# Optimization experiments

Hardware: AMD Instinct MI355X
Metric: run time of the kernel (lower is better)

## Reference

```python
import jax, jax.numpy as jnp
import numpy as np

MODES = 16
IN_CH = 64
OUT_CH = 64
SCALE = 1.0 / (IN_CH * OUT_CH)


def setup_inputs() -> dict:
    key = jax.random.key(0)
    k1, k2, k3 = jax.random.split(key, 3)
    v = jax.random.normal(k1, (32, IN_CH, 8192), dtype=jnp.float32)
    # torch.rand on cfloat -> uniform [0,1) real and imag parts, then scaled
    w_real = jax.random.uniform(k2, (MODES, OUT_CH, IN_CH), dtype=jnp.float32) * SCALE
    w_imag = jax.random.uniform(k3, (MODES, OUT_CH, IN_CH), dtype=jnp.float32) * SCALE
    return {"v": v, "w_real": w_real, "w_imag": w_imag}


def reference(v, w_real, w_imag):
    # v: [B, Cin, N]; weights: [modes, Cout, Cin] complex
    W = w_real + 1j * w_imag
    vf = jnp.fft.rfft(v)                      # [B, Cin, Nf], complex64
    nf = vf.shape[-1]
    # 'koi,bki->bko' with bki = vf[:,:, :modes] transposed -> equivalently:
    lv = jnp.einsum('koi,bik->bok', W, vf[:, :, :MODES])  # [B, Cout, modes]
    lv_full = jnp.pad(lv, ((0, 0), (0, 0), (0, nf - MODES)))  # zero high modes
    return jnp.fft.irfft(lv_full, n=v.shape[-1])  # [B, Cout, N] real
```

## Files before the change

kernel.cpp:

```cpp
#include <hip/hip_runtime.h>
#include <math.h>

#define NN 8192
#define NMODES 16
#define NB 32
#define NCH 64
#define NROWS (NB * NCH)
#define TPB 256

#define K8 0.70710678118654752440f

typedef float f32x4 __attribute__((ext_vector_type(4)));

struct KCTab { float c[16][4]; float s[16][4]; };
constexpr KCTab make_kc() {
  KCTab r{};
  for (int k = 0; k < 16; ++k)
    for (int c = 0; c < 4; ++c) {
      double th = 6.283185307179586476925287 * (double)(k * c) / 8192.0;
      double x2 = th * th;
      r.c[k][c] = (float)(1.0 - x2 / 2.0 + x2 * x2 / 24.0 - x2 * x2 * x2 / 720.0);
      r.s[k][c] = (float)(th - th * x2 / 6.0 + th * x2 * x2 / 120.0 - th * x2 * x2 * x2 / 5040.0);
    }
  return r;
}
constexpr KCTab KCT = make_kc();

__global__ __launch_bounds__(TPB) void fwd_dft_kernel(
    const float* __restrict__ v, float* __restrict__ vfpart) {
  const int row = blockIdx.x;
  const int t = threadIdx.x;
  const f32x4* __restrict__ vr4 = (const f32x4*)(v + (size_t)row * NN);

  float x[4][8];
#pragma unroll
  for (int j = 0; j < 8; ++j) {
    const f32x4 q = vr4[t + TPB * j];
    x[0][j] = q.x; x[1][j] = q.y; x[2][j] = q.z; x[3][j] = q.w;
  }

  float X0[4], X4[4], X1r[4], X1i[4], X2r[4], X2i[4], X3r[4], X3i[4];
#pragma unroll
  for (int c = 0; c < 4; ++c) {
    const float a  = x[c][0] + x[c][4], b = x[c][0] - x[c][4];
    const float cc = x[c][2] + x[c][6], d = x[c][2] - x[c][6];
    const float e  = x[c][1] + x[c][5], f = x[c][1] - x[c][5];
    const float g  = x[c][3] + x[c][7], h = x[c][3] - x[c][7];
    const float t1 = a + cc, t2 = e + g;
    X0[c]  = t1 + t2;
    X4[c]  = t1 - t2;
    X2r[c] = a - cc;  X2i[c] = g - e;
    const float u = K8 * (f - h), w = K8 * (f + h);
    X1r[c] = b + u;   X1i[c] = -d - w;
    X3r[c] = b - u;   X3i[c] = d - w;
  }

  double phi = (double)t * (6.283185307179586476925287 / 2048.0);
  double spd, cpd;
  sincos(phi, &spd, &cpd);
  const float c1 = (float)cpd, s1 = (float)spd;

  float pr[NMODES], pi[NMODES];
  float ck = 1.f, sk = 0.f;
#pragma unroll
  for (int k = 0; k < NMODES; ++k) {
    const int m = k & 7;
    float ar = 0.f, ai = 0.f;
#pragma unroll
    for (int c = 0; c < 4; ++c) {
      float br, bi;
      switch (m) {
        case 0:  br = X0[c];  bi = 0.f;      break;
        case 1:  br = X1r[c]; bi = X1i[c];   break;
        case 2:  br = X2r[c]; bi = X2i[c];   break;
        case 3:  br = X3r[c]; bi = X3i[c];   break;
        case 4:  br = X4[c];  bi = 0.f;      break;
        case 5:  br = X3r[c]; bi = -X3i[c];  break;
        case 6:  br = X2r[c]; bi = -X2i[c];  break;
        default: br = X1r[c]; bi = -X1i[c];  break;
      }
      if (c == 0) { ar = br; ai = bi; }
      else {
        ar = fmaf(br, KCT.c[k][c], fmaf(bi,  KCT.s[k][c], ar));
        ai = fmaf(bi, KCT.c[k][c], fmaf(br, -KCT.s[k][c], ai));
      }
    }
    pr[k] = ar * ck + ai * sk;
    pi[k] = ai * ck - ar * sk;
    const float cn = ck * c1 - sk * s1;
    const float sn = sk * c1 + ck * s1;
    ck = cn; sk = sn;
  }

  const int lane = t & 63, wave = t >> 6;

  float u16[16];
  {
    const bool hi = (lane & 16) != 0;
#pragma unroll
    for (int i = 0; i < 16; ++i) {
      const float send = hi ? pr[i] : pi[i];
      const float recv = __shfl_xor(send, 16);
      u16[i] = (hi ? pi[i] : pr[i]) + recv;
    }
  }
  float u8[8];
  {
    const bool hi = (lane & 8) != 0;
#pragma unroll
    for (int i = 0; i < 8; ++i) {
      const float send = hi ? u16[i] : u16[i + 8];
      const float recv = __shfl_xor(send, 8);
      u8[i] = (hi ? u16[i + 8] : u16[i]) + recv;
    }
  }
  float u4[4];
  {
    const bool hi = (lane & 4) != 0;
#pragma unroll
    for (int i = 0; i < 4; ++i) {
      const float send = hi ? u8[i] : u8[i + 4];
      const float recv = __shfl_xor(send, 4);
      u4[i] = (hi ? u8[i + 4] : u8[i]) + recv;
    }
  }
  float u2[2];
  {
    const bool hi = (lane & 2) != 0;
#pragma unroll
    for (int i = 0; i < 2; ++i) {
      const float send = hi ? u4[i] : u4[i + 2];
      const float recv = __shfl_xor(send, 2);
      u2[i] = (hi ? u4[i + 2] : u4[i]) + recv;
    }
  }
  float u1;
  {
    const bool hi = (lane & 1) != 0;
    const float send = hi ? u2[0] : u2[1];
    const float recv = __shfl_xor(send, 1);
    u1 = (hi ? u2[1] : u2[0]) + recv;
  }
  const float total = u1 + __shfl_xor(u1, 32);

  if (lane < 32) {
    vfpart[((size_t)row * 4 + wave) * 32 + lane] = total;
  }
}

__global__ __launch_bounds__(TPB) void mix_inv_kernel(
    const float* __restrict__ vfpart, const float* __restrict__ wre,
    const float* __restrict__ wim, float* __restrict__ out) {
  const int bid = blockIdx.x;
  const int b = bid >> 6, o = bid & 63;
  const int t = threadIdx.x;

  __shared__ float red[16][33];
  __shared__ float lvs[32];

  {
    const int k = t & 15, g = t >> 4;
    float lr = 0.f, li = 0.f;
#pragma unroll
    for (int ii = 0; ii < 4; ++ii) {
      const int i = g * 4 + ii;
      const float* __restrict__ p = vfpart + (size_t)(b * NCH + i) * 128;
      float vr = 0.f, vi = 0.f;
#pragma unroll
      for (int w = 0; w < 4; ++w) {
        vr += p[w * 32 + k];
        vi += p[w * 32 + 16 + k];
      }
      const float wr = wre[((size_t)k * NCH + o) * NCH + i];
      const float wi = wim[((size_t)k * NCH + o) * NCH + i];
      lr = fmaf(wr, vr, fmaf(-wi, vi, lr));
      li = fmaf(wr, vi, fmaf( wi, vr, li));
    }
    red[g][k]      = lr;
    red[g][16 + k] = li;
  }
  __syncthreads();
  if (t < 32) {
    float s = 0.f;
#pragma unroll
    for (int g = 0; g < 16; ++g) s += red[g][t];
    const float gk = ((t & 15) == 0) ? (1.0f / (float)NN) : (2.0f / (float)NN);
    lvs[t] = s * gk;
  }
  __syncthreads();

  double phi = (double)t * (6.283185307179586476925287 / 2048.0);
  double spd, cpd;
  sincos(phi, &spd, &cpd);
  const float c1 = (float)cpd, s1 = (float)spd;

  float Er[4][8], Ei[4][8];
  {
    float ck = 1.f, sk = 0.f;
#pragma unroll
    for (int k = 0; k < NMODES; ++k) {
      const int m = k & 7;
      const float Ar = lvs[k], Ai = lvs[16 + k];
      const float xr = Ar * ck - Ai * sk;
      const float xi = Ai * ck + Ar * sk;
      if (k < 8) { Er[0][m] = xr; Ei[0][m] = xi; }
      else       { Er[0][m] += xr; Ei[0][m] += xi; }
#pragma unroll
      for (int c = 1; c < 4; ++c) {
        const float dr = fmaf(xr, KCT.c[k][c], -xi * KCT.s[k][c]);
        const float di = fmaf(xi, KCT.c[k][c],  xr * KCT.s[k][c]);
        if (k < 8) { Er[c][m] = dr; Ei[c][m] = di; }
        else       { Er[c][m] += dr; Ei[c][m] += di; }
      }
      const float cn = ck * c1 - sk * s1;
      const float sn = sk * c1 + ck * s1;
      ck = cn; sk = sn;
    }
  }

  float y[4][8];
#pragma unroll
  for (int c = 0; c < 4; ++c) {
    const float P0 = Er[c][0], P4 = Er[c][4];
    const float P1 = Er[c][1] + Er[c][7], Q1 = Ei[c][1] - Ei[c][7];
    const float P2 = Er[c][2] + Er[c][6], Q2 = Ei[c][2] - Ei[c][6];
    const float P3 = Er[c][3] + Er[c][5], Q3 = Ei[c][3] - Ei[c][5];
    const float s04 = P0 + P4, d04 = P0 - P4;
    const float e0 = s04 + P2, e2 = s04 - P2;
    const float e1 = d04 - Q2, e3 = d04 + Q2;
    const float alpha = P1 - P3, beta = Q1 + Q3;
    const float O0 = P1 + P3;
    const float O2 = Q3 - Q1;
    const float O1 =  K8 * (alpha - beta);
    const float O3 = -K8 * (alpha + beta);
    y[c][0] = e0 + O0; y[c][4] = e0 - O0;
    y[c][1] = e1 + O1; y[c][5] = e1 - O1;
    y[c][2] = e2 + O2; y[c][6] = e2 - O2;
    y[c][3] = e3 + O3; y[c][7] = e3 - O3;
  }

  f32x4* __restrict__ out4 = (f32x4*)(out + (size_t)bid * NN);
#pragma unroll
  for (int j = 0; j < 8; ++j) {
    f32x4 r;
    r.x = y[0][j]; r.y = y[1][j]; r.z = y[2][j]; r.w = y[3][j];
    out4[t + TPB * j] = r;
  }
}

extern "C" void kernel_launch(void* const* d_in, const int* in_sizes, int n_in,
                              void* d_out, int out_size, void* d_ws, size_t ws_size,
                              hipStream_t stream) {
  const float* v   = (const float*)d_in[0];
  const float* wre = (const float*)d_in[1];
  const float* wim = (const float*)d_in[2];
  float* out = (float*)d_out;

  float* vfpart = (float*)d_ws;

  fwd_dft_kernel<<<NROWS, TPB, 0, stream>>>(v, vfpart);
  mix_inv_kernel<<<NROWS, TPB, 0, stream>>>(vfpart, wre, wim, out);
}
```

Before: 31.88 us.

## Split mode mixing into separate kernel before inverse DFT

Moves the channel-mixing contraction out of the fused mix+inverse kernel into its own small kernel (128 blocks, one thread per output channel and mode, looping over all 64 input channels), writing the mixed spectrum to a workspace buffer. The inverse DFT kernel then reads 32 floats per row directly instead of recomputing the mix with a shared-memory reduction and two barriers per block. This removes the redundant per-block reduction and barriers but adds a third kernel launch, a serial 64-step loop with strided weight loads, and a global round trip for the mixed spectrum.

```diff
diff --git a/kernel.cpp b/kernel.cpp
--- a/kernel.cpp
+++ b/kernel.cpp
@@ -148,46 +148,39 @@
   }
 }
 
-__global__ __launch_bounds__(TPB) void mix_inv_kernel(
+__global__ __launch_bounds__(256) void mix_kernel(
     const float* __restrict__ vfpart, const float* __restrict__ wre,
-    const float* __restrict__ wim, float* __restrict__ out) {
+    const float* __restrict__ wim, float* __restrict__ lv) {
+  const int k   = threadIdx.x & 15;
+  const int olo = threadIdx.x >> 4;
+  const int b   = blockIdx.x >> 2;
+  const int o   = (blockIdx.x & 3) * 16 + olo;
+
+  float lr = 0.f, li = 0.f;
+  for (int i = 0; i < NCH; ++i) {
+    const float* __restrict__ p = vfpart + (size_t)(b * NCH + i) * 128;
+    float vr = 0.f, vi = 0.f;
+#pragma unroll
+    for (int w = 0; w < 4; ++w) {
+      vr += p[w * 32 + k];
+      vi += p[w * 32 + 16 + k];
+    }
+    const float wr = wre[((size_t)k * NCH + o) * NCH + i];
+    const float wi = wim[((size_t)k * NCH + o) * NCH + i];
+    lr = fmaf(wr, vr, fmaf(-wi, vi, lr));
+    li = fmaf(wr, vi, fmaf( wi, vr, li));
+  }
+  const float gk = (k == 0) ? (1.0f / (float)NN) : (2.0f / (float)NN);
+  float* dst = lv + (size_t)(b * NCH + o) * 32;
+  dst[k]      = lr * gk;
+  dst[16 + k] = li * gk;
+}
+
+__global__ __launch_bounds__(TPB) void inv_kernel(
+    const float* __restrict__ lv, float* __restrict__ out) {
   const int bid = blockIdx.x;
-  const int b = bid >> 6, o = bid & 63;
   const int t = threadIdx.x;
-
-  __shared__ float red[16][33];
-  __shared__ float lvs[32];
-
-  {
-    const int k = t & 15, g = t >> 4;
-    float lr = 0.f, li = 0.f;
-#pragma unroll
-    for (int ii = 0; ii < 4; ++ii) {
-      const int i = g * 4 + ii;
-      const float* __restrict__ p = vfpart + (size_t)(b * NCH + i) * 128;
-      float vr = 0.f, vi = 0.f;
-#pragma unroll
-      for (int w = 0; w < 4; ++w) {
-        vr += p[w * 32 + k];
-        vi += p[w * 32 + 16 + k];
-      }
-      const float wr = wre[((size_t)k * NCH + o) * NCH + i];
-      const float wi = wim[((size_t)k * NCH + o) * NCH + i];
-      lr = fmaf(wr, vr, fmaf(-wi, vi, lr));
-      li = fmaf(wr, vi, fmaf( wi, vr, li));
-    }
-    red[g][k]      = lr;
-    red[g][16 + k] = li;
-  }
-  __syncthreads();
-  if (t < 32) {
-    float s = 0.f;
-#pragma unroll
-    for (int g = 0; g < 16; ++g) s += red[g][t];
-    const float gk = ((t & 15) == 0) ? (1.0f / (float)NN) : (2.0f / (float)NN);
-    lvs[t] = s * gk;
-  }
-  __syncthreads();
+  const float* __restrict__ L = lv + (size_t)bid * 32;
 
   double phi = (double)t * (6.283185307179586476925287 / 2048.0);
   double spd, cpd;
@@ -200,7 +193,7 @@
 #pragma unroll
     for (int k = 0; k < NMODES; ++k) {
       const int m = k & 7;
-      const float Ar = lvs[k], Ai = lvs[16 + k];
+      const float Ar = L[k], Ai = L[16 + k];
       const float xr = Ar * ck - Ai * sk;
       const float xi = Ai * ck + Ar * sk;
       if (k < 8) { Er[0][m] = xr; Ei[0][m] = xi; }
@@ -257,7 +250,9 @@
   float* out = (float*)d_out;
 
   float* vfpart = (float*)d_ws;
+  float* lvbuf  = vfpart + (size_t)NROWS * 4 * 32;
 
   fwd_dft_kernel<<<NROWS, TPB, 0, stream>>>(v, vfpart);
-  mix_inv_kernel<<<NROWS, TPB, 0, stream>>>(vfpart, wre, wim, out);
-}
+  mix_kernel<<<NB * 4, 256, 0, stream>>>(vfpart, wre, wim, lvbuf);
+  inv_kernel<<<NROWS, TPB, 0, stream>>>(lvbuf, out);
+}
```

New measurement: 46.13 us. 1.45x slower.

## Reduce wave partials in forward kernel and use shuffle reduction in mixing

Applied to the files above, without the earlier changes.

The forward DFT kernel now sums its four per-wave partial spectra in shared memory and writes one 32-float row, where before it wrote four partials per row. The mix kernel has a single wave load each channel's row with vector loads, form the 16 complex weight products per input channel, and reduce across channels with the shuffle tree. This removes one shared-memory reduction stage and a barrier, and cuts the number of partial reads. The cost is an added barrier in the forward kernel and three idle waves during the mixing step.

```diff
diff --git a/kernel.cpp b/kernel.cpp
--- a/kernel.cpp
+++ b/kernel.cpp
@@ -26,11 +26,67 @@
 }
 constexpr KCTab KCT = make_kc();
 
+__device__ __forceinline__ float reduce32(const float* a, const float* b, int lane) {
+  float u16[16];
+  {
+    const bool hi = (lane & 16) != 0;
+#pragma unroll
+    for (int i = 0; i < 16; ++i) {
+      const float send = hi ? a[i] : b[i];
+      const float recv = __shfl_xor(send, 16);
+      u16[i] = (hi ? b[i] : a[i]) + recv;
+    }
+  }
+  float u8[8];
+  {
+    const bool hi = (lane & 8) != 0;
+#pragma unroll
+    for (int i = 0; i < 8; ++i) {
+      const float send = hi ? u16[i] : u16[i + 8];
+      const float recv = __shfl_xor(send, 8);
+      u8[i] = (hi ? u16[i + 8] : u16[i]) + recv;
+    }
+  }
+  float u4[4];
+  {
+    const bool hi = (lane & 4) != 0;
+#pragma unroll
+    for (int i = 0; i < 4; ++i) {
+      const float send = hi ? u4[i] * 0.f + (hi ? u8[i] : u8[i + 4]) : u8[i + 4];
+      (void)send;
+      const float s2 = hi ? u8[i] : u8[i + 4];
+      const float recv = __shfl_xor(s2, 4);
+      u4[i] = (hi ? u8[i + 4] : u8[i]) + recv;
+    }
+  }
+  float u2[2];
+  {
+    const bool hi = (lane & 2) != 0;
+#pragma unroll
+    for (int i = 0; i < 2; ++i) {
+      const float s2 = hi ? u4[i] : u4[i + 2];
+      const float recv = __shfl_xor(s2, 2);
+      u2[i] = (hi ? u4[i + 2] : u4[i]) + recv;
+    }
+  }
+  float u1;
+  {
+    const bool hi = (lane & 1) != 0;
+    const float send = hi ? u2[0] : u2[1];
+    const float recv = __shfl_xor(send, 1);
+    u1 = (hi ? u2[1] : u2[0]) + recv;
+  }
+  return u1 + __shfl_xor(u1, 32);
+}
+
 __global__ __launch_bounds__(TPB) void fwd_dft_kernel(
-    const float* __restrict__ v, float* __restrict__ vfpart) {
+    const float* __restrict__ v, float* __restrict__ vfrow) {
   const int row = blockIdx.x;
   const int t = threadIdx.x;
+  const int lane = t & 63, wave = t >> 6;
   const f32x4* __restrict__ vr4 = (const f32x4*)(v + (size_t)row * NN);
+
+  __shared__ float red[4][32];
 
   float x[4][8];
 #pragma unroll
@@ -55,9 +111,9 @@
     X3r[c] = b - u;   X3i[c] = d - w;
   }
 
-  double phi = (double)t * (6.283185307179586476925287 / 2048.0);
+  double phid = (double)t * (6.283185307179586476925287 / 2048.0);
   double spd, cpd;
-  sincos(phi, &spd, &cpd);
+  sincos(phid, &spd, &cpd);
   const float c1 = (float)cpd, s1 = (float)spd;
 
   float pr[NMODES], pi[NMODES];
@@ -92,107 +148,59 @@
     ck = cn; sk = sn;
   }
 
-  const int lane = t & 63, wave = t >> 6;
-
-  float u16[16];
-  {
-    const bool hi = (lane & 16) != 0;
-#pragma unroll
-    for (int i = 0; i < 16; ++i) {
-      const float send = hi ? pr[i] : pi[i];
-      const float recv = __shfl_xor(send, 16);
-      u16[i] = (hi ? pi[i] : pr[i]) + recv;
-    }
-  }
-  float u8[8];
-  {
-    const bool hi = (lane & 8) != 0;
-#pragma unroll
-    for (int i = 0; i < 8; ++i) {
-      const float send = hi ? u16[i] : u16[i + 8];
-      const float recv = __shfl_xor(send, 8);
-      u8[i] = (hi ? u16[i + 8] : u16[i]) + recv;
-    }
-  }
-  float u4[4];
-  {
-    const bool hi = (lane & 4) != 0;
-#pragma unroll
-    for (int i = 0; i < 4; ++i) {
-      const float send = hi ? u8[i] : u8[i + 4];
-      const float recv = __shfl_xor(send, 4);
-      u4[i] = (hi ? u8[i + 4] : u8[i]) + recv;
-    }
-  }
-  float u2[2];
-  {
-    const bool hi = (lane & 2) != 0;
-#pragma unroll
-    for (int i = 0; i < 2; ++i) {
-      const float send = hi ? u4[i] : u4[i + 2];
-      const float recv = __shfl_xor(send, 2);
-      u2[i] = (hi ? u4[i + 2] : u4[i]) + recv;
-    }
-  }
-  float u1;
-  {
-    const bool hi = (lane & 1) != 0;
-    const float send = hi ? u2[0] : u2[1];
-    const float recv = __shfl_xor(send, 1);
-    u1 = (hi ? u2[1] : u2[0]) + recv;
-  }
-  const float total = u1 + __shfl_xor(u1, 32);
-
-  if (lane < 32) {
-    vfpart[((size_t)row * 4 + wave) * 32 + lane] = total;
+  const float total = reduce32(pr, pi, lane);
+
+  if (lane < 32) red[wave][lane] = total;
+  __syncthreads();
+  if (t < 32) {
+    vfrow[(size_t)row * 32 + t] = red[0][t] + red[1][t] + red[2][t] + red[3][t];
   }
 }
 
 __global__ __launch_bounds__(TPB) void mix_inv_kernel(
-    const float* __restrict__ vfpart, const float* __restrict__ wre,
+    const float* __restrict__ vfrow, const float* __restrict__ wre,
     const float* __restrict__ wim, float* __restrict__ out) {
   const int bid = blockIdx.x;
   const int b = bid >> 6, o = bid & 63;
   const int t = threadIdx.x;
-
-  __shared__ float red[16][33];
-  __shared__ float lvs[32];
-
-  {
-    const int k = t & 15, g = t >> 4;
-    float lr = 0.f, li = 0.f;
-#pragma unroll
-    for (int ii = 0; ii < 4; ++ii) {
-      const int i = g * 4 + ii;
-      const float* __restrict__ p = vfpart + (size_t)(b * NCH + i) * 128;
-      float vr = 0.f, vi = 0.f;
-#pragma unroll
-      for (int w = 0; w < 4; ++w) {
-        vr += p[w * 32 + k];
-        vi += p[w * 32 + 16 + k];
-      }
-      const float wr = wre[((size_t)k * NCH + o) * NCH + i];
-      const float wi = wim[((size_t)k * NCH + o) * NCH + i];
-      lr = fmaf(wr, vr, fmaf(-wi, vi, lr));
-      li = fmaf(wr, vi, fmaf( wi, vr, li));
-    }
-    red[g][k]      = lr;
-    red[g][16 + k] = li;
+  const int lane = t & 63, wave = t >> 6;
+
+  __shared__ float coef[32];
+
+  if (wave == 0) {
+    float VF[32];
+    const f32x4* __restrict__ src =
+        (const f32x4*)(vfrow + (size_t)(b * NCH + lane) * 32);
+#pragma unroll
+    for (int q = 0; q < 8; ++q) {
+      const f32x4 z = src[q];
+      VF[q * 4]     = z.x; VF[q * 4 + 1] = z.y;
+      VF[q * 4 + 2] = z.z; VF[q * 4 + 3] = z.w;
+    }
+
+    float lr[NMODES], li[NMODES];
+#pragma unroll
+    for (int k = 0; k < NMODES; ++k) {
+      const float wr = wre[((size_t)k * NCH + o) * NCH + lane];
+      const float wi = wim[((size_t)k * NCH + o) * NCH + lane];
+      lr[k] = fmaf(wr, VF[k], -wi * VF[16 + k]);
+      li[k] = fmaf(wr, VF[16 + k], wi * VF[k]);
+    }
+
+    const float tot = reduce32(lr, li, lane);
+    if (lane < 32) {
+      const float gk = ((lane & 15) == 0) ? (1.0f / (float)NN) : (2.0f / (float)NN);
+      coef[lane] = tot * gk;
+    }
   }
   __syncthreads();
-  if (t < 32) {
-    float s = 0.f;
-#pragma unroll
-    for (int g = 0; g < 16; ++g) s += red[g][t];
-    const float gk = ((t & 15) == 0) ? (1.0f / (float)NN) : (2.0f / (float)NN);
-    lvs[t] = s * gk;
-  }
-  __syncthreads();
-
-  double phi = (double)t * (6.283185307179586476925287 / 2048.0);
+
+  double phid = (double)t * (6.283185307179586476925287 / 2048.0);
   double spd, cpd;
-  sincos(phi, &spd, &cpd);
+  sincos(phid, &spd, &cpd);
   const float c1 = (float)cpd, s1 = (float)spd;
+
+  const float* __restrict__ L = coef;
 
   float Er[4][8], Ei[4][8];
   {
@@ -200,7 +208,7 @@
 #pragma unroll
     for (int k = 0; k < NMODES; ++k) {
       const int m = k & 7;
-      const float Ar = lvs[k], Ai = lvs[16 + k];
+      const float Ar = L[k], Ai = L[16 + k];
       const float xr = Ar * ck - Ai * sk;
       const float xi = Ai * ck + Ar * sk;
       if (k < 8) { Er[0][m] = xr; Ei[0][m] = xi; }
@@ -256,8 +264,8 @@
   const float* wim = (const float*)d_in[2];
   float* out = (float*)d_out;
 
-  float* vfpart = (float*)d_ws;
-
-  fwd_dft_kernel<<<NROWS, TPB, 0, stream>>>(v, vfpart);
-  mix_inv_kernel<<<NROWS, TPB, 0, stream>>>(vfpart, wre, wim, out);
-}
+  float* vfrow = (float*)d_ws;
+
+  fwd_dft_kernel<<<NROWS, TPB, 0, stream>>>(v, vfrow);
+  mix_inv_kernel<<<NROWS, TPB, 0, stream>>>(vfrow, wre, wim, out);
+}
```

Measured after the change: 34.73 us. 8.9% more time.
